# Kernel tuning notes

Measured on AMD Instinct MI355X. Metric: run time of the kernel, lower is better.

## Reference

```python
import jax, jax.numpy as jnp
import numpy as np

B, N_SRC, N_DST, E, F = 2, 131072, 131072, 524288, 64
EPS = 1e-8


def setup_inputs() -> dict:
    key = jax.random.key(0)
    k1, k2, k3 = jax.random.split(key, 3)
    x = jax.random.normal(k1, (B, N_SRC, F), dtype=jnp.float32)
    edge_index = jax.random.randint(k2, (2, E), 0, N_DST, dtype=jnp.int64)
    weights = jax.random.uniform(k3, (E,), dtype=jnp.float32)
    return {"x": x, "edge_index": edge_index, "weights": weights}


def reference(x, edge_index, weights):
    src = edge_index[0]  # (E,) indices into source nodes
    dst = edge_index[1]  # (E,) indices into destination nodes
    # _row_normalize_weights: normalize per destination node
    norm = jax.ops.segment_sum(weights, dst, num_segments=N_DST)  # (N_DST,)
    w = weights / (norm[dst] + EPS)  # (E,)
    # Batched SpMM: out[b, d, :] = sum_{e: dst[e]==d} w[e] * x[b, src[e], :]
    gathered = x[:, src, :] * w[None, :, None]  # (B, E, F)
    out = jnp.zeros((B, N_DST, F), dtype=x.dtype).at[:, dst, :].add(gathered)
    return out
```

## Files before the change

### kernel.cpp

```cpp
#include <hip/hip_runtime.h>

#define NB    2
#define NDST  131072
#define NSRC  131072
#define FF    64
#define EE    524288
#define EPSV  1e-8f

#define NBUCK  2048
#define NSEG   2
#define SEGCAP 224
#define CAPB   (NSEG * SEGCAP)
#define CPAD   32
#define NCUR   (NBUCK * NSEG)

typedef unsigned long long u64;

__global__ void init_kernel(int4* __restrict__ gcur4) {
    gcur4[blockIdx.x * 256 + threadIdx.x] = int4{0, 0, 0, 0};
}

__global__ __launch_bounds__(256) void scatter_kernel(const int* __restrict__ src,
                                                      const int* __restrict__ dst,
                                                      const float* __restrict__ wts,
                                                      int* __restrict__ gcur,
                                                      u64* __restrict__ rec) {
    int t   = threadIdx.x;
    int blk = blockIdx.x;
    int seg = blk & (NSEG - 1);
    int base = blk * 2048 + t;
    int d[8]; int s[8]; float w[8];
    #pragma unroll
    for (int i = 0; i < 8; ++i) {
        int e = base + i * 256;
        d[i] = __builtin_nontemporal_load(&dst[e]);
        s[i] = __builtin_nontemporal_load(&src[e]);
        w[i] = __builtin_nontemporal_load(&wts[e]);
    }
    int p[8];
    #pragma unroll
    for (int i = 0; i < 8; ++i) {
        int cell = (d[i] >> 6) * NSEG + seg;
        p[i] = atomicAdd(&gcur[cell << 5], 1);
    }
    #pragma unroll
    for (int i = 0; i < 8; ++i) {
        int cell = (d[i] >> 6) * NSEG + seg;
        u64 r = ((u64)__float_as_uint(w[i]) << 32)
              | ((u64)(d[i] & 63) << 17)
              | (unsigned)s[i];
        if (p[i] < SEGCAP)
            __builtin_nontemporal_store(r, &rec[(size_t)cell * SEGCAP + p[i]]);
    }
}

__global__ __launch_bounds__(256) void fused_kernel(const float* __restrict__ x,
                                                    const int* __restrict__ gcur,
                                                    const u64* __restrict__ rec,
                                                    float* __restrict__ out) {
    __shared__ u64 stage[CAPB];
    __shared__ u64 sorted[CAPB];
    __shared__ int cnt[64];
    __shared__ int loffs[65];

    int t = threadIdx.x;
    int k = blockIdx.x;
    int n0 = gcur[(k * NSEG + 0) << 5]; if (n0 > SEGCAP) n0 = SEGCAP;
    int n1 = gcur[(k * NSEG + 1) << 5]; if (n1 > SEGCAP) n1 = SEGCAP;
    const u64* __restrict__ b0 = rec + (size_t)(k * NSEG + 0) * SEGCAP;
    const u64* __restrict__ b1 = rec + (size_t)(k * NSEG + 1) * SEGCAP;
    int n = n0 + n1;

    if (t < 64) cnt[t] = 0;
    __syncthreads();

    for (int i = t; i < n0; i += 256) {
        u64 r = __builtin_nontemporal_load(&b0[i]);
        stage[i] = r;
        atomicAdd(&cnt[(int)((r >> 17) & 63)], 1);
    }
    for (int i = t; i < n1; i += 256) {
        u64 r = __builtin_nontemporal_load(&b1[i]);
        stage[n0 + i] = r;
        atomicAdd(&cnt[(int)((r >> 17) & 63)], 1);
    }
    __syncthreads();

    if (t < 64) {
        int c = cnt[t];
        int incl = c;
        #pragma unroll
        for (int off = 1; off < 64; off <<= 1) {
            int o = __shfl_up(incl, off, 64);
            if (t >= off) incl += o;
        }
        loffs[t + 1] = incl;
        if (t == 0) loffs[0] = 0;
        cnt[t] = incl - c;
    }
    __syncthreads();

    for (int i = t; i < n; i += 256) {
        u64 r = stage[i];
        int p = atomicAdd(&cnt[(int)((r >> 17) & 63)], 1);
        sorted[p] = r;
    }
    __syncthreads();

    int wave = t >> 6, lane = t & 63;
    int dlo = wave * 16, dhi = dlo + 16;
    int begin = loffs[dlo];
    int end   = loffs[dhi];
    const float* xb0 = x + lane;
    const float* xb1 = x + (size_t)NSRC * FF + lane;
    float* ob0 = out + lane + (size_t)(k * 64) * FF;
    float* ob1 = ob0 + (size_t)NDST * FF;

    float acc0 = 0.f, acc1 = 0.f, sumw = 0.f;
    int cur = dlo;

    for (int i = begin; i < end; i += 8) {
        int rem = end - i;
        u64 r[8];
        #pragma unroll
        for (int j = 0; j < 8; ++j)
            r[j] = (j < rem) ? sorted[i + j] : 0ULL;

        float a0[8], a1[8], w[8]; int bn[8];
        #pragma unroll
        for (int j = 0; j < 8; ++j) {
            int s  = (int)(r[j] & 0x1FFFF);
            w[j]   = __uint_as_float((unsigned)(r[j] >> 32));
            bn[j]  = (int)((r[j] >> 17) & 63);
            a0[j]  = xb0[(size_t)s * FF];
            a1[j]  = xb1[(size_t)s * FF];
        }
        #pragma unroll
        for (int j = 0; j < 8; ++j) {
            if (bn[j] > cur) {
                do {
                    float inv = 1.0f / (sumw + EPSV);
                    __builtin_nontemporal_store(acc0 * inv, &ob0[(size_t)cur * FF]);
                    __builtin_nontemporal_store(acc1 * inv, &ob1[(size_t)cur * FF]);
                    acc0 = 0.f; acc1 = 0.f; sumw = 0.f;
                    ++cur;
                } while (cur < bn[j]);
            }
            sumw += w[j];
            acc0 = fmaf(w[j], a0[j], acc0);
            acc1 = fmaf(w[j], a1[j], acc1);
        }
    }
    while (cur < dhi) {
        float inv = 1.0f / (sumw + EPSV);
        __builtin_nontemporal_store(acc0 * inv, &ob0[(size_t)cur * FF]);
        __builtin_nontemporal_store(acc1 * inv, &ob1[(size_t)cur * FF]);
        acc0 = 0.f; acc1 = 0.f; sumw = 0.f;
        ++cur;
    }
}

extern "C" void kernel_launch(void* const* d_in, const int* in_sizes, int n_in,
                              void* d_out, int out_size, void* d_ws, size_t ws_size,
                              hipStream_t stream) {
    const float* x          = (const float*)d_in[0];
    const int*   edge_index = (const int*)d_in[1];
    const float* weights    = (const float*)d_in[2];

    const int* src = edge_index;
    const int* dst = edge_index + EE;
    float* out = (float*)d_out;

    int* gcur = (int*)d_ws;
    u64* rec  = (u64*)((char*)d_ws + (size_t)NCUR * CPAD * sizeof(int));

    init_kernel<<<(NCUR * CPAD / 4) / 256, 256, 0, stream>>>((int4*)gcur);
    scatter_kernel<<<EE / 2048, 256, 0, stream>>>(src, dst, weights, gcur, rec);
    fused_kernel<<<NBUCK, 256, 0, stream>>>(x, gcur, rec, out);
}
```

Before: 177.9 us.

## Use float2 gathers per half-wave, smaller scatter tiles, drop nontemporal hints

The fused kernel now splits each wave into two half-waves, one per batch, and each lane loads and stores a float2. This replaces two scalar gathers per edge with one 8-byte vector gather. The scatter kernel processes 4 edges per thread instead of 8, launches twice as many blocks, and interleaves each atomic with its record store. Nontemporal load and store hints are removed from the scatter kernel and the record loads, which lets the records stay in cache between the two kernels but reduces memory-level parallelism per thread in scatter.

```diff
diff --git a/kernel.cpp b/kernel.cpp
--- a/kernel.cpp
+++ b/kernel.cpp
@@ -15,6 +15,7 @@
 #define NCUR   (NBUCK * NSEG)
 
 typedef unsigned long long u64;
+typedef __attribute__((ext_vector_type(2))) float fvec2;
 
 __global__ void init_kernel(int4* __restrict__ gcur4) {
     gcur4[blockIdx.x * 256 + threadIdx.x] = int4{0, 0, 0, 0};
@@ -28,29 +29,21 @@
     int t   = threadIdx.x;
     int blk = blockIdx.x;
     int seg = blk & (NSEG - 1);
-    int base = blk * 2048 + t;
-    int d[8]; int s[8]; float w[8];
+    int base = blk * 1024 + t;
+    int d[4]; int s[4]; float w[4];
     #pragma unroll
-    for (int i = 0; i < 8; ++i) {
+    for (int i = 0; i < 4; ++i) {
         int e = base + i * 256;
-        d[i] = __builtin_nontemporal_load(&dst[e]);
-        s[i] = __builtin_nontemporal_load(&src[e]);
-        w[i] = __builtin_nontemporal_load(&wts[e]);
-    }
-    int p[8];
-    #pragma unroll
-    for (int i = 0; i < 8; ++i) {
-        int cell = (d[i] >> 6) * NSEG + seg;
-        p[i] = atomicAdd(&gcur[cell << 5], 1);
+        d[i] = dst[e]; s[i] = src[e]; w[i] = wts[e];
     }
     #pragma unroll
-    for (int i = 0; i < 8; ++i) {
+    for (int i = 0; i < 4; ++i) {
         int cell = (d[i] >> 6) * NSEG + seg;
+        int p    = atomicAdd(&gcur[cell << 5], 1);
         u64 r = ((u64)__float_as_uint(w[i]) << 32)
               | ((u64)(d[i] & 63) << 17)
               | (unsigned)s[i];
-        if (p[i] < SEGCAP)
-            __builtin_nontemporal_store(r, &rec[(size_t)cell * SEGCAP + p[i]]);
+        if (p < SEGCAP) rec[(size_t)cell * SEGCAP + p] = r;
     }
 }
 
@@ -75,12 +68,12 @@
     __syncthreads();
 
     for (int i = t; i < n0; i += 256) {
-        u64 r = __builtin_nontemporal_load(&b0[i]);
+        u64 r = b0[i];
         stage[i] = r;
         atomicAdd(&cnt[(int)((r >> 17) & 63)], 1);
     }
     for (int i = t; i < n1; i += 256) {
-        u64 r = __builtin_nontemporal_load(&b1[i]);
+        u64 r = b1[i];
         stage[n0 + i] = r;
         atomicAdd(&cnt[(int)((r >> 17) & 63)], 1);
     }
@@ -108,15 +101,16 @@
     __syncthreads();
 
     int wave = t >> 6, lane = t & 63;
+    int half = lane >> 5;
+    int fl   = (lane & 31) * 2;
+    const float* __restrict__ xb = x + (size_t)half * NSRC * FF + fl;
+    float* ob = out + (size_t)half * NDST * FF + (size_t)(k * 64) * FF + fl;
+
     int dlo = wave * 16, dhi = dlo + 16;
     int begin = loffs[dlo];
     int end   = loffs[dhi];
-    const float* xb0 = x + lane;
-    const float* xb1 = x + (size_t)NSRC * FF + lane;
-    float* ob0 = out + lane + (size_t)(k * 64) * FF;
-    float* ob1 = ob0 + (size_t)NDST * FF;
 
-    float acc0 = 0.f, acc1 = 0.f, sumw = 0.f;
+    float ax = 0.f, ay = 0.f, sumw = 0.f;
     int cur = dlo;
 
     for (int i = begin; i < end; i += 8) {
@@ -126,36 +120,35 @@
         for (int j = 0; j < 8; ++j)
             r[j] = (j < rem) ? sorted[i + j] : 0ULL;
 
-        float a0[8], a1[8], w[8]; int bn[8];
+        fvec2 a[8]; float w[8]; int bn[8];
         #pragma unroll
         for (int j = 0; j < 8; ++j) {
-            int s  = (int)(r[j] & 0x1FFFF);
-            w[j]   = __uint_as_float((unsigned)(r[j] >> 32));
-            bn[j]  = (int)((r[j] >> 17) & 63);
-            a0[j]  = xb0[(size_t)s * FF];
-            a1[j]  = xb1[(size_t)s * FF];
+            int s = (int)(r[j] & 0x1FFFF);
+            w[j]  = __uint_as_float((unsigned)(r[j] >> 32));
+            bn[j] = (int)((r[j] >> 17) & 63);
+            a[j]  = *reinterpret_cast<const fvec2*>(&xb[(size_t)s * FF]);
         }
         #pragma unroll
         for (int j = 0; j < 8; ++j) {
             if (bn[j] > cur) {
                 do {
                     float inv = 1.0f / (sumw + EPSV);
-                    __builtin_nontemporal_store(acc0 * inv, &ob0[(size_t)cur * FF]);
-                    __builtin_nontemporal_store(acc1 * inv, &ob1[(size_t)cur * FF]);
-                    acc0 = 0.f; acc1 = 0.f; sumw = 0.f;
+                    fvec2 o; o.x = ax * inv; o.y = ay * inv;
+                    __builtin_nontemporal_store(o, reinterpret_cast<fvec2*>(&ob[(size_t)cur * FF]));
+                    ax = 0.f; ay = 0.f; sumw = 0.f;
                     ++cur;
                 } while (cur < bn[j]);
             }
             sumw += w[j];
-            acc0 = fmaf(w[j], a0[j], acc0);
-            acc1 = fmaf(w[j], a1[j], acc1);
+            ax = fmaf(w[j], a[j].x, ax);
+            ay = fmaf(w[j], a[j].y, ay);
         }
     }
     while (cur < dhi) {
         float inv = 1.0f / (sumw + EPSV);
-        __builtin_nontemporal_store(acc0 * inv, &ob0[(size_t)cur * FF]);
-        __builtin_nontemporal_store(acc1 * inv, &ob1[(size_t)cur * FF]);
-        acc0 = 0.f; acc1 = 0.f; sumw = 0.f;
+        fvec2 o; o.x = ax * inv; o.y = ay * inv;
+        __builtin_nontemporal_store(o, reinterpret_cast<fvec2*>(&ob[(size_t)cur * FF]));
+        ax = 0.f; ay = 0.f; sumw = 0.f;
         ++cur;
     }
 }
@@ -175,6 +168,6 @@
     u64* rec  = (u64*)((char*)d_ws + (size_t)NCUR * CPAD * sizeof(int));
 
     init_kernel<<<(NCUR * CPAD / 4) / 256, 256, 0, stream>>>((int4*)gcur);
-    scatter_kernel<<<EE / 2048, 256, 0, stream>>>(src, dst, weights, gcur, rec);
+    scatter_kernel<<<EE / 1024, 256, 0, stream>>>(src, dst, weights, gcur, rec);
     fused_kernel<<<NBUCK, 256, 0, stream>>>(x, gcur, rec, out);
 }
```

Result: faster. 170.4 us (-4.2%).
